# Kernel tuning notes

Measured on AMD Instinct MI355X. Metric: run time of the kernel, lower is better.

Reference implementation:

```python
import jax, jax.numpy as jnp
import numpy as np

VOCAB, EMBED, HIDDEN = 32000, 256, 512


def setup_inputs() -> dict:
    key = jax.random.key(0)
    ks = jax.random.split(key, 6)
    bound_ih = 1.0 / np.sqrt(EMBED)
    bound_hh = 1.0 / np.sqrt(HIDDEN)
    return {
        "input_seq": jax.random.randint(ks[0], (64, 512), 0, VOCAB, dtype=jnp.int64),
        "emb_table": jax.random.normal(ks[1], (VOCAB, EMBED), dtype=jnp.float32),
        "W_ih": jax.random.uniform(ks[2], (4 * HIDDEN, EMBED), jnp.float32, -bound_hh, bound_hh),
        "W_hh": jax.random.uniform(ks[3], (4 * HIDDEN, HIDDEN), jnp.float32, -bound_hh, bound_hh),
        "b_ih": jax.random.uniform(ks[4], (4 * HIDDEN,), jnp.float32, -bound_hh, bound_hh),
        "b_hh": jax.random.uniform(ks[5], (4 * HIDDEN,), jnp.float32, -bound_hh, bound_hh),
    }


def _lstm_forward(input_seq, emb_table, W_ih, W_hh, b_ih, b_hh):
    B, S = input_seq.shape
    H = W_hh.shape[1]
    # Embedding lookup for all timesteps: [B, S, E]
    emb = emb_table[input_seq]
    # Precompute input contribution to gates for all steps in one GEMM: [B, S, 4H]
    x_gates = jnp.einsum('bse,ge->bsg', emb, W_ih) + b_ih + b_hh
    x_gates = jnp.swapaxes(x_gates, 0, 1)  # [S, B, 4H] for scan

    def step(carry, xg):
        h, c = carry
        gates = xg + h @ W_hh.T  # [B, 4H]
        i, f, g, o = jnp.split(gates, 4, axis=-1)  # PyTorch LSTMCell gate order
        i = jax.nn.sigmoid(i)
        f = jax.nn.sigmoid(f)
        g = jnp.tanh(g)
        o = jax.nn.sigmoid(o)
        c = f * c + i * g
        h = o * jnp.tanh(c)
        return (h, c), None

    h0 = jnp.zeros((B, H), dtype=emb.dtype)
    c0 = jnp.zeros((B, H), dtype=emb.dtype)
    (h, c), _ = jax.lax.scan(step, (h0, c0), x_gates)
    return h, c


def reference(input_seq, emb_table, W_ih, W_hh, b_ih, b_hh):
    return _lstm_forward(input_seq, emb_table, W_ih, W_hh, b_ih, b_hh)
```

## Files before the change

kernel.cpp:

```cpp
#include <hip/hip_runtime.h>


typedef _Float16 half2_t __attribute__((ext_vector_type(2)));
typedef _Float16 half8 __attribute__((ext_vector_type(8)));
typedef float f32x4 __attribute__((ext_vector_type(4)));
typedef short short4_t __attribute__((ext_vector_type(4)));

__device__ __forceinline__ float dot2h(int w, int h, float c) {
#if __has_builtin(__builtin_amdgcn_fdot2)
  return __builtin_amdgcn_fdot2(__builtin_bit_cast(half2_t, w),
                                __builtin_bit_cast(half2_t, h), c, false);
#else
  half2_t a = __builtin_bit_cast(half2_t, w);
  half2_t b = __builtin_bit_cast(half2_t, h);
  return fmaf((float)a[1], (float)b[1], fmaf((float)a[0], (float)b[0], c));
#endif
}

__device__ __forceinline__ float sigm(float x) { return 1.0f / (1.0f + __expf(-x)); }
__device__ __forceinline__ float tanh_(float x) { return 1.0f - 2.0f / (__expf(2.0f * x) + 1.0f); }

template <int OFF>
__device__ __forceinline__ int4 ld_c16o(const void* p) {
  int4 v;
  asm volatile("global_load_dwordx4 %0, %1, off offset:%2 sc0 sc1"
               : "=v"(v) : "v"(p), "i"(OFF) : "memory");
  return v;
}

__global__ __launch_bounds__(256) void prep_kernel(
    const float* __restrict__ W_hh, const float* __restrict__ W_ih,
    const float* __restrict__ b_ih, const float* __restrict__ b_hh,
    _Float16* __restrict__ Wd, _Float16* __restrict__ Wip,
    float* __restrict__ bsum, _Float16* __restrict__ Hz,
    float* __restrict__ cstate, unsigned* __restrict__ flags) {
  const int S0 = 1048576;
  const int S1 = S0 + 65536;
  const int S2 = S1 + 2048;
  const int S3 = S2 + 65536;
  const int S4 = S3 + 32768;
  const int S5 = S4 + 1024;
  for (int idx = blockIdx.x * blockDim.x + threadIdx.x; idx < S5;
       idx += gridDim.x * blockDim.x) {
    if (idx < S0) {
      int k = idx & 511, row = (idx >> 9) & 31, blk = idx >> 14;
      int u = row >> 2, g = row & 3;
      Wd[idx] = (_Float16)W_hh[(size_t)(g * 512 + blk * 8 + u) * 512 + k];
    } else if (idx < S1) {
      int e = idx - S0;
      int j = e & 511, k2 = e >> 9;
#pragma unroll
      for (int g = 0; g < 4; ++g) {
        Wip[(size_t)(k2 * 512 + j) * 8 + g * 2 + 0] =
            (_Float16)W_ih[(size_t)(g * 512 + j) * 256 + 2 * k2 + 0];
        Wip[(size_t)(k2 * 512 + j) * 8 + g * 2 + 1] =
            (_Float16)W_ih[(size_t)(g * 512 + j) * 256 + 2 * k2 + 1];
      }
    } else if (idx < S2) {
      int e = idx - S1;
      int j = e >> 2, g = e & 3;
      bsum[e] = b_ih[g * 512 + j] + b_hh[g * 512 + j];
    } else if (idx < S3) {
      Hz[idx - S2] = (_Float16)0.0f;
    } else if (idx < S4) {
      cstate[idx - S3] = 0.0f;
    } else {
      flags[idx - S4] = 0u;
    }
  }
}

__global__ __launch_bounds__(512, 1) void xg_kernel(
    const int* __restrict__ seq, const float* __restrict__ emb,
    const _Float16* __restrict__ Wip, const float* __restrict__ bsum,
    _Float16* __restrict__ xg, int t0, int Tc) {
  __shared__ int toks[8];
  __shared__ __align__(16) _Float16 el[128 * 16];
  const int tid = threadIdx.x;
  const int tau0 = blockIdx.x * 8;

  if (tid < 8) {
    int tau = tau0 + tid;
    int b = tau / Tc, tl = tau - b * Tc;
    toks[tid] = seq[b * 512 + t0 + tl];
  }
  __syncthreads();
  for (int e = tid; e < 2048; e += 512) {
    int i = e >> 8, k = e & 255;
    el[((k >> 1) * 8 + i) * 2 + (k & 1)] = (_Float16)emb[(size_t)toks[i] * 256 + k];
  }
  __syncthreads();

  const int j = tid;
  float4 bs = *(const float4*)&bsum[j * 4];
  float acc[8][4];
#pragma unroll
  for (int i = 0; i < 8; ++i) {
    acc[i][0] = bs.x; acc[i][1] = bs.y; acc[i][2] = bs.z; acc[i][3] = bs.w;
  }
  const _Float16* wp = Wip + (size_t)j * 8;
#pragma unroll 2
  for (int k2 = 0; k2 < 128; ++k2) {
    int4 w = *(const int4*)(wp + (size_t)k2 * 4096);
    int4 e0 = *(const int4*)(el + k2 * 16);
    int4 e1 = *(const int4*)(el + k2 * 16 + 8);
    acc[0][0] = dot2h(w.x, e0.x, acc[0][0]); acc[0][1] = dot2h(w.y, e0.x, acc[0][1]);
    acc[0][2] = dot2h(w.z, e0.x, acc[0][2]); acc[0][3] = dot2h(w.w, e0.x, acc[0][3]);
    acc[1][0] = dot2h(w.x, e0.y, acc[1][0]); acc[1][1] = dot2h(w.y, e0.y, acc[1][1]);
    acc[1][2] = dot2h(w.z, e0.y, acc[1][2]); acc[1][3] = dot2h(w.w, e0.y, acc[1][3]);
    acc[2][0] = dot2h(w.x, e0.z, acc[2][0]); acc[2][1] = dot2h(w.y, e0.z, acc[2][1]);
    acc[2][2] = dot2h(w.z, e0.z, acc[2][2]); acc[2][3] = dot2h(w.w, e0.z, acc[2][3]);
    acc[3][0] = dot2h(w.x, e0.w, acc[3][0]); acc[3][1] = dot2h(w.y, e0.w, acc[3][1]);
    acc[3][2] = dot2h(w.z, e0.w, acc[3][2]); acc[3][3] = dot2h(w.w, e0.w, acc[3][3]);
    acc[4][0] = dot2h(w.x, e1.x, acc[4][0]); acc[4][1] = dot2h(w.y, e1.x, acc[4][1]);
    acc[4][2] = dot2h(w.z, e1.x, acc[4][2]); acc[4][3] = dot2h(w.w, e1.x, acc[4][3]);
    acc[5][0] = dot2h(w.x, e1.y, acc[5][0]); acc[5][1] = dot2h(w.y, e1.y, acc[5][1]);
    acc[5][2] = dot2h(w.z, e1.y, acc[5][2]); acc[5][3] = dot2h(w.w, e1.y, acc[5][3]);
    acc[6][0] = dot2h(w.x, e1.z, acc[6][0]); acc[6][1] = dot2h(w.y, e1.z, acc[6][1]);
    acc[6][2] = dot2h(w.z, e1.z, acc[6][2]); acc[6][3] = dot2h(w.w, e1.z, acc[6][3]);
    acc[7][0] = dot2h(w.x, e1.w, acc[7][0]); acc[7][1] = dot2h(w.y, e1.w, acc[7][1]);
    acc[7][2] = dot2h(w.z, e1.w, acc[7][2]); acc[7][3] = dot2h(w.w, e1.w, acc[7][3]);
  }
#pragma unroll
  for (int i = 0; i < 8; ++i) {
    short4_t sv;
    sv[0] = __builtin_bit_cast(short, (_Float16)acc[i][0]);
    sv[1] = __builtin_bit_cast(short, (_Float16)acc[i][1]);
    sv[2] = __builtin_bit_cast(short, (_Float16)acc[i][2]);
    sv[3] = __builtin_bit_cast(short, (_Float16)acc[i][3]);
    *(short4_t*)(xg + ((size_t)(tau0 + i) * 512 + j) * 4) = sv;
  }
}

__global__ __launch_bounds__(256, 1) void rec3_kernel(
    const _Float16* __restrict__ xg, const _Float16* __restrict__ Wd,
    _Float16* __restrict__ H0, _Float16* __restrict__ H1,
    float* __restrict__ cstate, unsigned* __restrict__ flags,
    float* __restrict__ out, int t0, int Tc) {
  const int blk = blockIdx.x;
  const int tid = threadIdx.x;
  const int l = tid & 63, w = tid >> 6;
  const int lm = l & 15, koct = l >> 4;
  const int pb = w * 16 + lm;
  const int j0 = blk * 8 + koct;
  const int j1 = j0 + 4;

  half8 Af0[16], Af1[16];
  {
    const _Float16* a0 = Wd + ((size_t)blk * 32 + lm) * 512 + koct * 8;
    const _Float16* a1 = a0 + 16 * 512;
#pragma unroll
    for (int kk = 0; kk < 16; ++kk) {
      Af0[kk] = *(const half8*)(a0 + kk * 32);
      Af1[kk] = *(const half8*)(a1 + kk * 32);
    }
  }

  float c0 = cstate[pb * 512 + j0];
  float c1 = cstate[pb * 512 + j1];

  for (int tl = 0; tl < Tc; ++tl) {
    const int t = t0 + tl;
    const _Float16* Hc = (t & 1) ? H1 : H0;
    _Float16* Hn = (t & 1) ? H0 : H1;

    const _Float16* hb = Hc + (size_t)pb * 512 + koct * 8;
    int4 bhv[16];
    bhv[0] = ld_c16o<0>(hb);    bhv[1] = ld_c16o<64>(hb);
    bhv[2] = ld_c16o<128>(hb);  bhv[3] = ld_c16o<192>(hb);
    bhv[4] = ld_c16o<256>(hb);  bhv[5] = ld_c16o<320>(hb);
    bhv[6] = ld_c16o<384>(hb);  bhv[7] = ld_c16o<448>(hb);
    bhv[8] = ld_c16o<512>(hb);  bhv[9] = ld_c16o<576>(hb);
    bhv[10] = ld_c16o<640>(hb); bhv[11] = ld_c16o<704>(hb);
    bhv[12] = ld_c16o<768>(hb); bhv[13] = ld_c16o<832>(hb);
    bhv[14] = ld_c16o<896>(hb); bhv[15] = ld_c16o<960>(hb);
    short4_t xs0 = *(const short4_t*)(xg + ((size_t)(pb * Tc + tl) * 512 + j0) * 4);
    short4_t xs1 = *(const short4_t*)(xg + ((size_t)(pb * Tc + tl) * 512 + j1) * 4);
    asm volatile("s_waitcnt vmcnt(0)" ::: "memory");
    __builtin_amdgcn_sched_barrier(0);

    f32x4 ac0 = {0.f, 0.f, 0.f, 0.f}, ac1 = {0.f, 0.f, 0.f, 0.f};
#pragma unroll
    for (int kk = 0; kk < 16; ++kk) {
      half8 B = __builtin_bit_cast(half8, bhv[kk]);
      ac0 = __builtin_amdgcn_mfma_f32_16x16x32_f16(Af0[kk], B, ac0, 0, 0, 0);
      ac1 = __builtin_amdgcn_mfma_f32_16x16x32_f16(Af1[kk], B, ac1, 0, 0, 0);
    }

    float G0 = (float)__builtin_bit_cast(_Float16, (short)xs0[0]) + ac0[0];
    float G1 = (float)__builtin_bit_cast(_Float16, (short)xs0[1]) + ac0[1];
    float G2 = (float)__builtin_bit_cast(_Float16, (short)xs0[2]) + ac0[2];
    float G3 = (float)__builtin_bit_cast(_Float16, (short)xs0[3]) + ac0[3];
    float ig = sigm(G0), fg = sigm(G1), gg = tanh_(G2), og = sigm(G3);
    c0 = fg * c0 + ig * gg;
    float hn0 = og * tanh_(c0);

    G0 = (float)__builtin_bit_cast(_Float16, (short)xs1[0]) + ac1[0];
    G1 = (float)__builtin_bit_cast(_Float16, (short)xs1[1]) + ac1[1];
    G2 = (float)__builtin_bit_cast(_Float16, (short)xs1[2]) + ac1[2];
    G3 = (float)__builtin_bit_cast(_Float16, (short)xs1[3]) + ac1[3];
    float ig1 = sigm(G0), fg1 = sigm(G1), gg1 = tanh_(G2), og1 = sigm(G3);
    c1 = fg1 * c1 + ig1 * gg1;
    float hn1 = og1 * tanh_(c1);

    unsigned hb0 = (unsigned)__builtin_bit_cast(unsigned short, (_Float16)hn0);
    unsigned hb1 = (unsigned)__builtin_bit_cast(unsigned short, (_Float16)hn1);
    unsigned nb0 = (unsigned)__shfl_xor((int)hb0, 16, 64);
    unsigned nb1 = (unsigned)__shfl_xor((int)hb1, 16, 64);
    if ((koct & 1) == 0) {
      unsigned* bse = (unsigned*)(Hn + (size_t)pb * 512 + blk * 8);
      __hip_atomic_store(bse + (koct >> 1), hb0 | (nb0 << 16),
                         __ATOMIC_RELAXED, __HIP_MEMORY_SCOPE_AGENT);
      __hip_atomic_store(bse + 2 + (koct >> 1), hb1 | (nb1 << 16),
                         __ATOMIC_RELAXED, __HIP_MEMORY_SCOPE_AGENT);
    }
    if (t == 511) {
      out[pb * 512 + j0] = hn0; out[32768 + pb * 512 + j0] = c0;
      out[pb * 512 + j1] = hn1; out[32768 + pb * 512 + j1] = c1;
    }

    if (tl != Tc - 1) {
      asm volatile("s_waitcnt vmcnt(0)" ::: "memory");
      __syncthreads();
      if (tid == 0)
        __hip_atomic_store(flags + blk * 16, (unsigned)(t + 1),
                           __ATOMIC_RELAXED, __HIP_MEMORY_SCOPE_AGENT);
      if (w == 0) {
        const unsigned tgt = (unsigned)(t + 1);
        while (true) {
          unsigned f;
          asm volatile("global_load_dword %0, %1, off sc0 sc1"
                       : "=v"(f) : "v"(flags + l * 16) : "memory");
          asm volatile("s_waitcnt vmcnt(0)" ::: "memory");
          if (__all((int)(f >= tgt))) break;
          __builtin_amdgcn_s_sleep(1);
        }
      }
      __syncthreads();
    }
  }
  cstate[pb * 512 + j0] = c0;
  cstate[pb * 512 + j1] = c1;
}

__global__ __launch_bounds__(512, 1) void naive_kernel(
    const int* __restrict__ seq, const float* __restrict__ emb,
    const float* __restrict__ W_ih, const float* __restrict__ W_hh,
    const float* __restrict__ b_ih, const float* __restrict__ b_hh,
    float* __restrict__ out) {
  __shared__ float hl[512];
  const int b = blockIdx.x, j = threadIdx.x;
  hl[j] = 0.f;
  float c = 0.f;
  __syncthreads();
  for (int t = 0; t < 512; ++t) {
    int tok = seq[b * 512 + t];
    float A[4];
#pragma unroll
    for (int g = 0; g < 4; ++g) A[g] = b_ih[g * 512 + j] + b_hh[g * 512 + j];
    for (int k = 0; k < 256; ++k) {
      float e = emb[(size_t)tok * 256 + k];
#pragma unroll
      for (int g = 0; g < 4; ++g) A[g] += e * W_ih[(size_t)(g * 512 + j) * 256 + k];
    }
    for (int k = 0; k < 512; ++k) {
      float h = hl[k];
#pragma unroll
      for (int g = 0; g < 4; ++g) A[g] += h * W_hh[(size_t)(g * 512 + j) * 512 + k];
    }
    __syncthreads();
    float ig = sigm(A[0]), fg = sigm(A[1]), gg = tanh_(A[2]), og = sigm(A[3]);
    c = fg * c + ig * gg;
    float hn = og * tanh_(c);
    hl[j] = hn;
    __syncthreads();
    if (t == 511) {
      out[b * 512 + j] = hn;
      out[32768 + b * 512 + j] = c;
    }
  }
}

extern "C" void kernel_launch(void* const* d_in, const int* in_sizes, int n_in,
                              void* d_out, int out_size, void* d_ws, size_t ws_size,
                              hipStream_t stream) {
  const int* seq = (const int*)d_in[0];
  const float* emb = (const float*)d_in[1];
  const float* W_ih = (const float*)d_in[2];
  const float* W_hh = (const float*)d_in[3];
  const float* b_ih = (const float*)d_in[4];
  const float* b_hh = (const float*)d_in[5];
  float* out = (float*)d_out;

  char* w = (char*)d_ws;
  _Float16* Wd = (_Float16*)(w + 0);
  _Float16* Wip = (_Float16*)(w + 2097152);
  float* bsum = (float*)(w + 3145728);
  _Float16* H0 = (_Float16*)(w + 3153920);
  _Float16* H1 = (_Float16*)(w + 3219456);
  float* cstate = (float*)(w + 3284992);
  unsigned* flags = (unsigned*)(w + 3416064);
  _Float16* xgbuf = (_Float16*)(w + 3420160);
  const size_t base = 3420160;

  int Tc = 0;
  const int cands[7] = {512, 256, 128, 64, 32, 16, 8};
  for (int ci = 0; ci < 7; ++ci) {
    if (base + (size_t)cands[ci] * 262144 <= ws_size) { Tc = cands[ci]; break; }
  }

  if (Tc == 0) {
    naive_kernel<<<64, 512, 0, stream>>>(seq, emb, W_ih, W_hh, b_ih, b_hh, out);
    return;
  }

  prep_kernel<<<1024, 256, 0, stream>>>(W_hh, W_ih, b_ih, b_hh, Wd, Wip, bsum,
                                        H0, cstate, flags);
  for (int t0 = 0; t0 < 512; t0 += Tc) {
    xg_kernel<<<8 * Tc, 512, 0, stream>>>(seq, emb, Wip, bsum, xgbuf, t0, Tc);
    rec3_kernel<<<64, 256, 0, stream>>>(xgbuf, Wd, H0, H1, cstate, flags, out,
                                        t0, Tc);
  }
}
```

Baseline: 2.691 ms.

## Replace grid barrier with per-chunk dataflow flags and triple-buffered hidden state

The full grid barrier after every timestep is removed. Each block now polls the 64 per-block flags and, as soon as all four producer blocks covering a 64-column slice of h have published step t, loads that slice and issues its MFMAs. This overlaps waiting with partial compute. A third hidden-state buffer (rotating mod 3) prevents fast blocks from overwriting data slower blocks still read, and the flags are packed contiguously. The trade-offs are more polling traffic and branchy, partially serialized MFMA issue. Correctness depends on the rotating-buffer and flag-ordering reasoning holding across kernel launches.

```diff
diff --git a/kernel.cpp b/kernel.cpp
--- a/kernel.cpp
+++ b/kernel.cpp
@@ -37,9 +37,9 @@
   const int S0 = 1048576;
   const int S1 = S0 + 65536;
   const int S2 = S1 + 2048;
-  const int S3 = S2 + 65536;
+  const int S3 = S2 + 32768;
   const int S4 = S3 + 32768;
-  const int S5 = S4 + 1024;
+  const int S5 = S4 + 64;
   for (int idx = blockIdx.x * blockDim.x + threadIdx.x; idx < S5;
        idx += gridDim.x * blockDim.x) {
     if (idx < S0) {
@@ -134,9 +134,8 @@
 
 __global__ __launch_bounds__(256, 1) void rec3_kernel(
     const _Float16* __restrict__ xg, const _Float16* __restrict__ Wd,
-    _Float16* __restrict__ H0, _Float16* __restrict__ H1,
-    float* __restrict__ cstate, unsigned* __restrict__ flags,
-    float* __restrict__ out, int t0, int Tc) {
+    _Float16* __restrict__ H, float* __restrict__ cstate,
+    unsigned* __restrict__ flags, float* __restrict__ out, int t0, int Tc) {
   const int blk = blockIdx.x;
   const int tid = threadIdx.x;
   const int l = tid & 63, w = tid >> 6;
@@ -159,32 +158,57 @@
   float c0 = cstate[pb * 512 + j0];
   float c1 = cstate[pb * 512 + j1];
 
+  int rc = t0 % 3;
+
   for (int tl = 0; tl < Tc; ++tl) {
     const int t = t0 + tl;
-    const _Float16* Hc = (t & 1) ? H1 : H0;
-    _Float16* Hn = (t & 1) ? H0 : H1;
+    const _Float16* Hc = H + (size_t)rc * 32768;
+    const int wc = (rc == 2) ? 0 : rc + 1;
+    _Float16* Hn = H + (size_t)wc * 32768;
+
+    short4_t xs0 = *(const short4_t*)(xg + ((size_t)(pb * Tc + tl) * 512 + j0) * 4);
+    short4_t xs1 = *(const short4_t*)(xg + ((size_t)(pb * Tc + tl) * 512 + j1) * 4);
 
     const _Float16* hb = Hc + (size_t)pb * 512 + koct * 8;
     int4 bhv[16];
-    bhv[0] = ld_c16o<0>(hb);    bhv[1] = ld_c16o<64>(hb);
-    bhv[2] = ld_c16o<128>(hb);  bhv[3] = ld_c16o<192>(hb);
-    bhv[4] = ld_c16o<256>(hb);  bhv[5] = ld_c16o<320>(hb);
-    bhv[6] = ld_c16o<384>(hb);  bhv[7] = ld_c16o<448>(hb);
-    bhv[8] = ld_c16o<512>(hb);  bhv[9] = ld_c16o<576>(hb);
-    bhv[10] = ld_c16o<640>(hb); bhv[11] = ld_c16o<704>(hb);
-    bhv[12] = ld_c16o<768>(hb); bhv[13] = ld_c16o<832>(hb);
-    bhv[14] = ld_c16o<896>(hb); bhv[15] = ld_c16o<960>(hb);
-    short4_t xs0 = *(const short4_t*)(xg + ((size_t)(pb * Tc + tl) * 512 + j0) * 4);
-    short4_t xs1 = *(const short4_t*)(xg + ((size_t)(pb * Tc + tl) * 512 + j1) * 4);
-    asm volatile("s_waitcnt vmcnt(0)" ::: "memory");
-    __builtin_amdgcn_sched_barrier(0);
-
     f32x4 ac0 = {0.f, 0.f, 0.f, 0.f}, ac1 = {0.f, 0.f, 0.f, 0.f};
-#pragma unroll
-    for (int kk = 0; kk < 16; ++kk) {
-      half8 B = __builtin_bit_cast(half8, bhv[kk]);
-      ac0 = __builtin_amdgcn_mfma_f32_16x16x32_f16(Af0[kk], B, ac0, 0, 0, 0);
-      ac1 = __builtin_amdgcn_mfma_f32_16x16x32_f16(Af1[kk], B, ac1, 0, 0, 0);
+    const unsigned tgt = (unsigned)t;
+    unsigned done = 0;
+    while (done != 0xFFFFu) {
+      unsigned f;
+      asm volatile("global_load_dword %0, %1, off sc0 sc1"
+                   : "=v"(f) : "v"(flags + l) : "memory");
+      asm volatile("s_waitcnt vmcnt(0)" ::: "memory");
+      unsigned long long rdy = __ballot((int)(f >= tgt));
+      unsigned newly = 0;
+#define TRYLOAD(KK)                                                          \
+  if (!((done >> KK) & 1u) && (((rdy >> (4 * KK)) & 0xFull) == 0xFull)) {    \
+    bhv[KK] = ld_c16o<KK * 64>(hb);                                          \
+    newly |= (1u << KK);                                                     \
+  }
+      TRYLOAD(0) TRYLOAD(1) TRYLOAD(2) TRYLOAD(3)
+      TRYLOAD(4) TRYLOAD(5) TRYLOAD(6) TRYLOAD(7)
+      TRYLOAD(8) TRYLOAD(9) TRYLOAD(10) TRYLOAD(11)
+      TRYLOAD(12) TRYLOAD(13) TRYLOAD(14) TRYLOAD(15)
+#undef TRYLOAD
+      if (newly) {
+        asm volatile("s_waitcnt vmcnt(0)" ::: "memory");
+        __builtin_amdgcn_sched_barrier(0);
+#define DOMFMA(KK)                                                           \
+  if ((newly >> KK) & 1u) {                                                  \
+    half8 B = __builtin_bit_cast(half8, bhv[KK]);                            \
+    ac0 = __builtin_amdgcn_mfma_f32_16x16x32_f16(Af0[KK], B, ac0, 0, 0, 0);  \
+    ac1 = __builtin_amdgcn_mfma_f32_16x16x32_f16(Af1[KK], B, ac1, 0, 0, 0);  \
+  }
+        DOMFMA(0) DOMFMA(1) DOMFMA(2) DOMFMA(3)
+        DOMFMA(4) DOMFMA(5) DOMFMA(6) DOMFMA(7)
+        DOMFMA(8) DOMFMA(9) DOMFMA(10) DOMFMA(11)
+        DOMFMA(12) DOMFMA(13) DOMFMA(14) DOMFMA(15)
+#undef DOMFMA
+        done |= newly;
+      } else {
+        __builtin_amdgcn_s_sleep(1);
+      }
     }
 
     float G0 = (float)__builtin_bit_cast(_Float16, (short)xs0[0]) + ac0[0];
@@ -203,15 +227,15 @@
     c1 = fg1 * c1 + ig1 * gg1;
     float hn1 = og1 * tanh_(c1);
 
-    unsigned hb0 = (unsigned)__builtin_bit_cast(unsigned short, (_Float16)hn0);
-    unsigned hb1 = (unsigned)__builtin_bit_cast(unsigned short, (_Float16)hn1);
-    unsigned nb0 = (unsigned)__shfl_xor((int)hb0, 16, 64);
-    unsigned nb1 = (unsigned)__shfl_xor((int)hb1, 16, 64);
+    unsigned hq0 = (unsigned)__builtin_bit_cast(unsigned short, (_Float16)hn0);
+    unsigned hq1 = (unsigned)__builtin_bit_cast(unsigned short, (_Float16)hn1);
+    unsigned nq0 = (unsigned)__shfl_xor((int)hq0, 16, 64);
+    unsigned nq1 = (unsigned)__shfl_xor((int)hq1, 16, 64);
     if ((koct & 1) == 0) {
       unsigned* bse = (unsigned*)(Hn + (size_t)pb * 512 + blk * 8);
-      __hip_atomic_store(bse + (koct >> 1), hb0 | (nb0 << 16),
+      __hip_atomic_store(bse + (koct >> 1), hq0 | (nq0 << 16),
                          __ATOMIC_RELAXED, __HIP_MEMORY_SCOPE_AGENT);
-      __hip_atomic_store(bse + 2 + (koct >> 1), hb1 | (nb1 << 16),
+      __hip_atomic_store(bse + 2 + (koct >> 1), hq1 | (nq1 << 16),
                          __ATOMIC_RELAXED, __HIP_MEMORY_SCOPE_AGENT);
     }
     if (t == 511) {
@@ -219,25 +243,12 @@
       out[pb * 512 + j1] = hn1; out[32768 + pb * 512 + j1] = c1;
     }
 
-    if (tl != Tc - 1) {
-      asm volatile("s_waitcnt vmcnt(0)" ::: "memory");
-      __syncthreads();
-      if (tid == 0)
-        __hip_atomic_store(flags + blk * 16, (unsigned)(t + 1),
-                           __ATOMIC_RELAXED, __HIP_MEMORY_SCOPE_AGENT);
-      if (w == 0) {
-        const unsigned tgt = (unsigned)(t + 1);
-        while (true) {
-          unsigned f;
-          asm volatile("global_load_dword %0, %1, off sc0 sc1"
-                       : "=v"(f) : "v"(flags + l * 16) : "memory");
-          asm volatile("s_waitcnt vmcnt(0)" ::: "memory");
-          if (__all((int)(f >= tgt))) break;
-          __builtin_amdgcn_s_sleep(1);
-        }
-      }
-      __syncthreads();
-    }
+    asm volatile("s_waitcnt vmcnt(0)" ::: "memory");
+    __syncthreads();
+    if (tid == 0)
+      __hip_atomic_store(flags + blk, (unsigned)(t + 1), __ATOMIC_RELAXED,
+                         __HIP_MEMORY_SCOPE_AGENT);
+    rc = wc;
   }
   cstate[pb * 512 + j0] = c0;
   cstate[pb * 512 + j1] = c1;
@@ -296,12 +307,11 @@
   _Float16* Wd = (_Float16*)(w + 0);
   _Float16* Wip = (_Float16*)(w + 2097152);
   float* bsum = (float*)(w + 3145728);
-  _Float16* H0 = (_Float16*)(w + 3153920);
-  _Float16* H1 = (_Float16*)(w + 3219456);
-  float* cstate = (float*)(w + 3284992);
-  unsigned* flags = (unsigned*)(w + 3416064);
-  _Float16* xgbuf = (_Float16*)(w + 3420160);
-  const size_t base = 3420160;
+  _Float16* H = (_Float16*)(w + 3153920);
+  float* cstate = (float*)(w + 3350528);
+  unsigned* flags = (unsigned*)(w + 3481600);
+  _Float16* xgbuf = (_Float16*)(w + 3485696);
+  const size_t base = 3485696;
 
   int Tc = 0;
   const int cands[7] = {512, 256, 128, 64, 32, 16, 8};
@@ -315,10 +325,10 @@
   }
 
   prep_kernel<<<1024, 256, 0, stream>>>(W_hh, W_ih, b_ih, b_hh, Wd, Wip, bsum,
-                                        H0, cstate, flags);
+                                        H, cstate, flags);
   for (int t0 = 0; t0 < 512; t0 += Tc) {
     xg_kernel<<<8 * Tc, 512, 0, stream>>>(seq, emb, Wip, bsum, xgbuf, t0, Tc);
-    rec3_kernel<<<64, 256, 0, stream>>>(xgbuf, Wd, H0, H1, cstate, flags, out,
+    rec3_kernel<<<64, 256, 0, stream>>>(xgbuf, Wd, H, cstate, flags, out,
                                         t0, Tc);
   }
 }
```

Result: slower. 3.065 ms (+13.9%).
